# Kernel optimization log

Hardware: AMD Instinct MI355X
Metric: run time of the kernel (lower is better)

The kernel has to match this reference:

```python
import jax, jax.numpy as jnp
import numpy as np

K = 16            # fixed number of clusters (labels in [0, K))
ALPHA = 1.0
BETA = 1.0
GAMMA = 0.001
VAR_THETA = 0.5
DIST_THETA = 1.5


def setup_inputs() -> dict:
    key = jax.random.key(0)
    k1, k2 = jax.random.split(key)
    B, D, H, W = 8, 32, 512, 512
    embeddings = jax.random.normal(k1, (B, D, H, W), dtype=jnp.float32)
    g_truths = jax.random.randint(k2, (B, H, W), 0, K, dtype=jnp.int32)
    return {"embeddings": embeddings, "g_truths": g_truths}


def _per_image_loss(emb, gt):
    # emb: [D, H, W], gt: [H, W] int32
    D = emb.shape[0]
    x = emb.reshape(D, -1).T              # [N, D] pixels
    lbl = gt.reshape(-1)                  # [N]

    counts = jax.ops.segment_sum(jnp.ones_like(lbl, dtype=x.dtype), lbl, num_segments=K)  # [K]
    counts = jnp.maximum(counts, 1.0)
    sums = jax.ops.segment_sum(x, lbl, num_segments=K)                                    # [K, D]
    means = sums / counts[:, None]                                                        # [K, D]

    # variance (pull) loss: per-cluster mean of hinge^2 on distance to cluster mean
    d2 = jnp.sum((x - means[lbl]) ** 2, axis=-1)         # [N]
    hinge = jnp.maximum(jnp.sqrt(d2) - VAR_THETA, 0.0) ** 2
    per_cluster = jax.ops.segment_sum(hinge, lbl, num_segments=K) / counts
    variance_loss = jnp.mean(per_cluster)

    # distance (push) loss over unordered pairs i<j, normalized by K*(K-1)
    diffs = means[:, None, :] - means[None, :, :]        # [K, K, D]
    sq = jnp.sum(diffs ** 2, axis=-1) + jnp.eye(K, dtype=x.dtype)  # eye guards sqrt(0) on diag
    pd = jnp.sqrt(sq)
    hinge_pd = jnp.maximum(2.0 * DIST_THETA - pd, 0.0) ** 2
    upper = jnp.triu(jnp.ones((K, K), dtype=x.dtype), k=1)
    distance_loss = jnp.sum(hinge_pd * upper) / (K * (K - 1))

    # regularization: mean L2 norm of cluster means
    reg_loss = jnp.mean(jnp.linalg.norm(means, axis=1))

    return ALPHA * variance_loss + BETA * distance_loss + GAMMA * reg_loss


def reference(embeddings, g_truths):
    losses = jax.vmap(_per_image_loss)(embeddings, g_truths)  # [B]
    return jnp.mean(losses)
```

## Files before the change

kernel.cpp:

```cpp
#include <hip/hip_runtime.h>

#define B_IMG 8
#define D_DIM 32
#define NPIX 262144
#define K_CL 16

#define CHUNK_S 4096
#define CHUNKS_S (NPIX / CHUNK_S)
#define AST 257

#define CHUNK_V 1024
#define CHUNKS_V (NPIX / CHUNK_V)
#define VST 264

__device__ __forceinline__ float wave_sum(float v) {
#pragma unroll
  for (int off = 32; off > 0; off >>= 1) v += __shfl_xor(v, off, 64);
  return v;
}

template <int NC>
__device__ __forceinline__ float4 wave_sum4(float4 v) {
#pragma unroll
  for (int off = 32; off > 0; off >>= 1) {
    v.x += __shfl_xor(v.x, off, 64);
    if (NC == 4) {
      v.y += __shfl_xor(v.y, off, 64);
      v.z += __shfl_xor(v.z, off, 64);
      v.w += __shfl_xor(v.w, off, 64);
    }
  }
  return v;
}

template <int NC>
__device__ __forceinline__ void flush4(float4 (*acc)[AST], int tid,
                                       float* base, int rstride) {
  const int w = tid >> 6, lane = tid & 63;
#pragma unroll
  for (int rr = 0; rr < 4; rr++) {
    const int r = (w << 2) | rr;
    float4 s = make_float4(0.f, 0.f, 0.f, 0.f);
#pragma unroll
    for (int q = 0; q < 4; q++) {
      float4 v = acc[r][(q << 6) | lane];
      acc[r][(q << 6) | lane] = make_float4(0.f, 0.f, 0.f, 0.f);
      s.x += v.x; s.y += v.y; s.z += v.z; s.w += v.w;
    }
    s = wave_sum4<NC>(s);
    if (lane == 0) {
      unsafeAtomicAdd(base + r * rstride + 0, s.x);
      if (NC == 4) {
        unsafeAtomicAdd(base + r * rstride + 1, s.y);
        unsafeAtomicAdd(base + r * rstride + 2, s.z);
        unsafeAtomicAdd(base + r * rstride + 3, s.w);
      }
    }
  }
}

__global__ __launch_bounds__(256) void k_sums(const float* __restrict__ emb,
                                              const int* __restrict__ gt,
                                              float* __restrict__ sums,
                                              float* __restrict__ counts) {
  __shared__ float4 acc4[K_CL][AST];
  const int tid = threadIdx.x;
  const int b = blockIdx.x >> 6;
  const int chunk = blockIdx.x & (CHUNKS_S - 1);
  const int base = chunk * CHUNK_S;

  int lb[16];
  {
    const int4* lp = (const int4*)(gt + (size_t)b * NPIX + base);
#pragma unroll
    for (int h = 0; h < 4; h++) {
      int4 a = lp[tid + (h << 8)];
      lb[h * 4 + 0] = a.x; lb[h * 4 + 1] = a.y;
      lb[h * 4 + 2] = a.z; lb[h * 4 + 3] = a.w;
    }
  }
#pragma unroll
  for (int k = 0; k < K_CL; k++) acc4[k][tid] = make_float4(0.f, 0.f, 0.f, 0.f);
  __syncthreads();

#pragma unroll
  for (int j = 0; j < 16; j++) acc4[lb[j]][tid].x += 1.0f;
  __syncthreads();
  flush4<1>(acc4, tid, counts + b * K_CL, 1);
  __syncthreads();

  for (int g = 0; g < 8; g++) {
    const float* eb = emb + ((size_t)b * D_DIM + g * 4) * NPIX + base;
#pragma unroll
    for (int h = 0; h < 4; h++) {
      float4 v[4];
#pragma unroll
      for (int d = 0; d < 4; d++)
        v[d] = ((const float4*)(eb + (size_t)d * NPIX))[tid + (h << 8)];
#pragma unroll
      for (int c = 0; c < 4; c++) {
        const int l = lb[h * 4 + c];
        float4 t;
        t.x = ((const float*)&v[0])[c];
        t.y = ((const float*)&v[1])[c];
        t.z = ((const float*)&v[2])[c];
        t.w = ((const float*)&v[3])[c];
        float4 old = acc4[l][tid];
        old.x += t.x; old.y += t.y; old.z += t.z; old.w += t.w;
        acc4[l][tid] = old;
      }
    }
    __syncthreads();
    flush4<4>(acc4, tid, sums + (size_t)b * K_CL * D_DIM + g * 4, D_DIM);
    __syncthreads();
  }
}

__global__ __launch_bounds__(256) void k_var(const float* __restrict__ emb,
                                             const int* __restrict__ gt,
                                             const float* __restrict__ sums,
                                             const float* __restrict__ counts,
                                             float* __restrict__ var_sums,
                                             float* __restrict__ dist_reg) {
  __shared__ float acc[K_CL][VST];
  __shared__ float4 mk4[K_CL][9];
  __shared__ float msq[K_CL];
  __shared__ float red4[4];
  const int tid = threadIdx.x;
  const int b = blockIdx.x >> 8;
  const int chunk = blockIdx.x & (CHUNKS_V - 1);
  const int base = chunk * CHUNK_V;

  float* mkf = (float*)mk4;
#pragma unroll
  for (int e0 = 0; e0 < 2; e0++) {
    const int e = tid + (e0 << 8);
    const int k = e >> 5, d = e & 31;
    const float c = fmaxf(counts[b * K_CL + k], 1.0f);
    mkf[k * 36 + d] = sums[(size_t)b * K_CL * D_DIM + e] / c;
  }
#pragma unroll
  for (int k = 0; k < K_CL; k++) acc[k][tid] = 0.f;
  __syncthreads();
  if (tid < K_CL) {
    float s = 0.f;
#pragma unroll
    for (int g = 0; g < 8; g++) {
      float4 m = mk4[tid][g];
      s = fmaf(m.x, m.x, s); s = fmaf(m.y, m.y, s);
      s = fmaf(m.z, m.z, s); s = fmaf(m.w, m.w, s);
    }
    msq[tid] = s;
  }
  __syncthreads();

  if (chunk == 0) {
    const int i = tid >> 4, j = tid & 15;
    float sq = 0.f;
#pragma unroll
    for (int g = 0; g < 8; g++) {
      float4 mi = mk4[i][g], mj = mk4[j][g];
      float dx = mi.x - mj.x, dy = mi.y - mj.y, dz = mi.z - mj.z, dw = mi.w - mj.w;
      sq = fmaf(dx, dx, sq); sq = fmaf(dy, dy, sq);
      sq = fmaf(dz, dz, sq); sq = fmaf(dw, dw, sq);
    }
    float contrib = 0.f;
    if (i < j) {
      const float h = fmaxf(3.0f - sqrtf(sq), 0.0f);
      contrib = h * h;
    }
    const float tot = wave_sum(contrib);
    if ((tid & 63) == 0) red4[tid >> 6] = tot;
    __syncthreads();
    if (tid == 0) {
      const float dist = (red4[0] + red4[1] + red4[2] + red4[3]) * (1.0f / 240.0f);
      float reg = 0.f;
#pragma unroll
      for (int k = 0; k < K_CL; k++) reg += sqrtf(msq[k]);
      dist_reg[b] = dist + 0.001f * (reg * (1.0f / 16.0f));
    }
  }

  int lb[4];
  {
    const int4* lp = (const int4*)(gt + (size_t)b * NPIX + base);
    int4 a = lp[tid];
    lb[0] = a.x; lb[1] = a.y; lb[2] = a.z; lb[3] = a.w;
  }
  float a[4] = {0.f, 0.f, 0.f, 0.f};

#pragma unroll 2
  for (int g = 0; g < 8; g++) {
    const float* eb = emb + ((size_t)b * D_DIM + g * 4) * NPIX + base;
    float4 v[4];
#pragma unroll
    for (int d = 0; d < 4; d++)
      v[d] = ((const float4*)(eb + (size_t)d * NPIX))[tid];
#pragma unroll
    for (int j = 0; j < 4; j++) {
      const float4 m4 = mk4[lb[j]][g];
#pragma unroll
      for (int d = 0; d < 4; d++) {
        const float x = ((const float*)&v[d])[j];
        const float mm = ((const float*)&m4)[d];
        a[j] = fmaf(x, x - 2.0f * mm, a[j]);
      }
    }
  }
#pragma unroll
  for (int j = 0; j < 4; j++) {
    const float d2 = a[j] + msq[lb[j]];
    const float dd = sqrtf(fmaxf(d2, 0.f));
    const float h = fmaxf(dd - 0.5f, 0.f);
    acc[lb[j]][tid] += h * h;
  }
  __syncthreads();

  const int w = tid >> 6, lane = tid & 63;
#pragma unroll
  for (int rr = 0; rr < 4; rr++) {
    const int r = (w << 2) | rr;
    float4 vv = *(float4*)(&acc[r][lane << 2]);
    float tot = wave_sum(vv.x + vv.y + vv.z + vv.w);
    if (lane == 0) unsafeAtomicAdd(&var_sums[b * K_CL + r], tot);
  }
}

__global__ __launch_bounds__(128) void k_final(const float* __restrict__ counts,
                                               const float* __restrict__ var_sums,
                                               const float* __restrict__ dist_reg,
                                               float* __restrict__ out) {
  const int t = threadIdx.x;
  float pc = 0.f;
  if (t < B_IMG * K_CL) pc = var_sums[t] / fmaxf(counts[t], 1.0f);
#pragma unroll
  for (int off = 8; off > 0; off >>= 1) pc += __shfl_xor(pc, off, 64);
  __shared__ float lbl[B_IMG];
  if (t < B_IMG * K_CL && (t & 15) == 0) {
    const int b = t >> 4;
    lbl[b] = pc * (1.0f / 16.0f) + dist_reg[b];
  }
  __syncthreads();
  if (t == 0) {
    float s = 0.f;
#pragma unroll
    for (int b = 0; b < B_IMG; b++) s += lbl[b];
    out[0] = s * (1.0f / B_IMG);
  }
}

extern "C" void kernel_launch(void* const* d_in, const int* in_sizes, int n_in,
                              void* d_out, int out_size, void* d_ws, size_t ws_size,
                              hipStream_t stream) {
  const float* emb = (const float*)d_in[0];
  const int* gt = (const int*)d_in[1];
  float* out = (float*)d_out;

  float* sums = (float*)d_ws;
  float* counts = sums + B_IMG * K_CL * D_DIM;
  float* var_sums = counts + B_IMG * K_CL;
  float* dist_reg = var_sums + B_IMG * K_CL;

  const size_t ws_floats = B_IMG * K_CL * D_DIM + 2 * B_IMG * K_CL + B_IMG;
  hipMemsetAsync(d_ws, 0, ws_floats * sizeof(float), stream);

  k_sums<<<dim3(B_IMG * CHUNKS_S), dim3(256), 0, stream>>>(emb, gt, sums, counts);
  k_var<<<dim3(B_IMG * CHUNKS_V), dim3(256), 0, stream>>>(emb, gt, sums, counts,
                                                          var_sums, dist_reg);
  k_final<<<dim3(1), dim3(128), 0, stream>>>(counts, var_sums, dist_reg, out);
}
```

Measured before the change: 573.6 us.

## Restructure segment-sum kernel to per-dimension scalar LDS accumulators with smaller chunks

The sums kernel now accumulates one embedding dimension at a time into a scalar shared-memory array (16 x 272 floats) instead of 4-wide float4 accumulators. The chunk per block is halved, doubling the grid to 1024 blocks, with 8 pixels per thread. This shrinks LDS use and register pressure for better occupancy and simpler flushes, but adds 32 barrier-and-flush rounds per block (one per dimension) instead of 8, and doubles the number of global atomics.

```diff
diff --git a/kernel.cpp b/kernel.cpp
--- a/kernel.cpp
+++ b/kernel.cpp
@@ -5,9 +5,10 @@
 #define NPIX 262144
 #define K_CL 16
 
-#define CHUNK_S 4096
+#define CHUNK_S 2048
 #define CHUNKS_S (NPIX / CHUNK_S)
-#define AST 257
+#define PPT 8
+#define ACC_STRIDE 272
 
 #define CHUNK_V 1024
 #define CHUNKS_V (NPIX / CHUNK_V)
@@ -19,43 +20,16 @@
   return v;
 }
 
-template <int NC>
-__device__ __forceinline__ float4 wave_sum4(float4 v) {
-#pragma unroll
-  for (int off = 32; off > 0; off >>= 1) {
-    v.x += __shfl_xor(v.x, off, 64);
-    if (NC == 4) {
-      v.y += __shfl_xor(v.y, off, 64);
-      v.z += __shfl_xor(v.z, off, 64);
-      v.w += __shfl_xor(v.w, off, 64);
-    }
-  }
-  return v;
-}
-
-template <int NC>
-__device__ __forceinline__ void flush4(float4 (*acc)[AST], int tid,
-                                       float* base, int rstride) {
+__device__ __forceinline__ void flush_acc(float (*acc)[ACC_STRIDE], int tid,
+                                          float* target, int stride) {
   const int w = tid >> 6, lane = tid & 63;
 #pragma unroll
   for (int rr = 0; rr < 4; rr++) {
     const int r = (w << 2) | rr;
-    float4 s = make_float4(0.f, 0.f, 0.f, 0.f);
-#pragma unroll
-    for (int q = 0; q < 4; q++) {
-      float4 v = acc[r][(q << 6) | lane];
-      acc[r][(q << 6) | lane] = make_float4(0.f, 0.f, 0.f, 0.f);
-      s.x += v.x; s.y += v.y; s.z += v.z; s.w += v.w;
-    }
-    s = wave_sum4<NC>(s);
-    if (lane == 0) {
-      unsafeAtomicAdd(base + r * rstride + 0, s.x);
-      if (NC == 4) {
-        unsafeAtomicAdd(base + r * rstride + 1, s.y);
-        unsafeAtomicAdd(base + r * rstride + 2, s.z);
-        unsafeAtomicAdd(base + r * rstride + 3, s.w);
-      }
-    }
+    float4 v = *(float4*)(&acc[r][lane << 2]);
+    *(float4*)(&acc[r][lane << 2]) = make_float4(0.f, 0.f, 0.f, 0.f);
+    float tot = wave_sum(v.x + v.y + v.z + v.w);
+    if (lane == 0) unsafeAtomicAdd(&target[r * stride], tot);
   }
 }
 
@@ -63,55 +37,39 @@
                                               const int* __restrict__ gt,
                                               float* __restrict__ sums,
                                               float* __restrict__ counts) {
-  __shared__ float4 acc4[K_CL][AST];
+  __shared__ alignas(16) float acc[K_CL][ACC_STRIDE];
   const int tid = threadIdx.x;
-  const int b = blockIdx.x >> 6;
+  const int b = blockIdx.x >> 7;
   const int chunk = blockIdx.x & (CHUNKS_S - 1);
   const int base = chunk * CHUNK_S;
 
-  int lb[16];
+  int lb[PPT];
   {
     const int4* lp = (const int4*)(gt + (size_t)b * NPIX + base);
-#pragma unroll
-    for (int h = 0; h < 4; h++) {
-      int4 a = lp[tid + (h << 8)];
-      lb[h * 4 + 0] = a.x; lb[h * 4 + 1] = a.y;
-      lb[h * 4 + 2] = a.z; lb[h * 4 + 3] = a.w;
-    }
-  }
-#pragma unroll
-  for (int k = 0; k < K_CL; k++) acc4[k][tid] = make_float4(0.f, 0.f, 0.f, 0.f);
-  __syncthreads();
-
-#pragma unroll
-  for (int j = 0; j < 16; j++) acc4[lb[j]][tid].x += 1.0f;
-  __syncthreads();
-  flush4<1>(acc4, tid, counts + b * K_CL, 1);
-  __syncthreads();
-
-  for (int g = 0; g < 8; g++) {
-    const float* eb = emb + ((size_t)b * D_DIM + g * 4) * NPIX + base;
-#pragma unroll
-    for (int h = 0; h < 4; h++) {
-      float4 v[4];
-#pragma unroll
-      for (int d = 0; d < 4; d++)
-        v[d] = ((const float4*)(eb + (size_t)d * NPIX))[tid + (h << 8)];
-#pragma unroll
-      for (int c = 0; c < 4; c++) {
-        const int l = lb[h * 4 + c];
-        float4 t;
-        t.x = ((const float*)&v[0])[c];
-        t.y = ((const float*)&v[1])[c];
-        t.z = ((const float*)&v[2])[c];
-        t.w = ((const float*)&v[3])[c];
-        float4 old = acc4[l][tid];
-        old.x += t.x; old.y += t.y; old.z += t.z; old.w += t.w;
-        acc4[l][tid] = old;
-      }
-    }
+    int4 a0 = lp[tid];
+    int4 a1 = lp[256 + tid];
+    lb[0] = a0.x; lb[1] = a0.y; lb[2] = a0.z; lb[3] = a0.w;
+    lb[4] = a1.x; lb[5] = a1.y; lb[6] = a1.z; lb[7] = a1.w;
+  }
+#pragma unroll
+  for (int k = 0; k < K_CL; k++) acc[k][tid] = 0.f;
+  __syncthreads();
+
+#pragma unroll
+  for (int j = 0; j < PPT; j++) acc[lb[j]][tid] += 1.0f;
+  __syncthreads();
+  flush_acc(acc, tid, counts + b * K_CL, 1);
+  __syncthreads();
+
+  for (int d = 0; d < D_DIM; d++) {
+    const float4* pp = (const float4*)(emb + ((size_t)b * D_DIM + d) * NPIX + base);
+    alignas(16) float v[PPT];
+    *(float4*)&v[0] = pp[tid];
+    *(float4*)&v[4] = pp[256 + tid];
+#pragma unroll
+    for (int j = 0; j < PPT; j++) acc[lb[j]][tid] += v[j];
     __syncthreads();
-    flush4<4>(acc4, tid, sums + (size_t)b * K_CL * D_DIM + g * 4, D_DIM);
+    flush_acc(acc, tid, sums + (size_t)b * K_CL * D_DIM + d, D_DIM);
     __syncthreads();
   }
 }
@@ -183,8 +141,7 @@
 
   int lb[4];
   {
-    const int4* lp = (const int4*)(gt + (size_t)b * NPIX + base);
-    int4 a = lp[tid];
+    const int4 a = ((const int4*)(gt + (size_t)b * NPIX + base))[tid];
     lb[0] = a.x; lb[1] = a.y; lb[2] = a.z; lb[3] = a.w;
   }
   float a[4] = {0.f, 0.f, 0.f, 0.f};
@@ -262,7 +219,7 @@
   float* dist_reg = var_sums + B_IMG * K_CL;
 
   const size_t ws_floats = B_IMG * K_CL * D_DIM + 2 * B_IMG * K_CL + B_IMG;
-  hipMemsetAsync(d_ws, 0, ws_floats * sizeof(float), stream);
+  (void)hipMemsetAsync(d_ws, 0, ws_floats * sizeof(float), stream);
 
   k_sums<<<dim3(B_IMG * CHUNKS_S), dim3(256), 0, stream>>>(emb, gt, sums, counts);
   k_var<<<dim3(B_IMG * CHUNKS_V), dim3(256), 0, stream>>>(emb, gt, sums, counts,
```

After: 598.7 us. +4.4%, slower.
